# Optimization experiments

Measured on AMD Instinct MI355X. Metric: run time of the kernel, lower is better.

## Reference

```python
import jax, jax.numpy as jnp
import numpy as np

H = 64  # hidden size
IN = 4  # input size


def _lstm_cell(h, c, xt, w_ih, w_hh, b):
    # PyTorch gate order: i, f, g, o
    gates = xt @ w_ih.T + h @ w_hh.T + b  # [B, 4H]
    i, f, g, o = jnp.split(gates, 4, axis=-1)
    i = jax.nn.sigmoid(i)
    f = jax.nn.sigmoid(f)
    g = jnp.tanh(g)
    o = jax.nn.sigmoid(o)
    c = f * c + i * g
    h = o * jnp.tanh(c)
    return h, c


def setup_inputs() -> dict:
    key = jax.random.key(0)
    ks = jax.random.split(key, 12)
    B, T = 512, 1000
    s = 1.0 / np.sqrt(H)  # PyTorch LSTM/Linear init scale
    u = lambda k, shape: jax.random.uniform(k, shape, jnp.float32, -s, s)
    return {
        "x": jax.random.normal(ks[0], (B, T, IN), jnp.float32),
        "w_ih_f": u(ks[1], (4 * H, IN)),
        "w_hh_f": u(ks[2], (4 * H, H)),
        "b_ih_f": u(ks[3], (4 * H,)),
        "b_hh_f": u(ks[4], (4 * H,)),
        "w_ih_b": u(ks[5], (4 * H, IN)),
        "w_hh_b": u(ks[6], (4 * H, H)),
        "b_ih_b": u(ks[7], (4 * H,)),
        "b_hh_b": u(ks[8], (4 * H,)),
        "w_fc": u(ks[9], (1, 2 * H)),
        "b_fc": u(ks[10], (1,)),
    }


def reference(x, w_ih_f, w_hh_f, b_ih_f, b_hh_f,
              w_ih_b, w_hh_b, b_ih_b, b_hh_b, w_fc, b_fc):
    B = x.shape[0]
    # Forward-direction LSTM: only the final hidden state is consumed
    # (out[:, -1, :64] == h_fwd after the last step).
    b_f = b_ih_f + b_hh_f

    def step(carry, xt):
        h, c = carry
        h, c = _lstm_cell(h, c, xt, w_ih_f, w_hh_f, b_f)
        return (h, c), None

    init = (jnp.zeros((B, H), x.dtype), jnp.zeros((B, H), x.dtype))
    xs = jnp.swapaxes(x, 0, 1)  # [T, B, IN]
    (h_fwd, _), _ = jax.lax.scan(step, init, xs)

    # Backward-direction output at the LAST timestep is the backward LSTM's
    # FIRST step (it processes the sequence reversed from zero state):
    # out[:, -1, 64:] == cell(0, 0, x[:, -1]).
    b_b = b_ih_b + b_hh_b
    h0 = jnp.zeros((B, H), x.dtype)
    h_bwd, _ = _lstm_cell(h0, h0, x[:, -1, :], w_ih_b, w_hh_b, b_b)

    last = jnp.concatenate([h_fwd, h_bwd], axis=-1)  # [B, 128]
    # Dropout is identity in eval mode.
    logits = last @ w_fc.T + b_fc  # [B, 1]
    return jax.nn.sigmoid(logits)[:, 0]
```

## Files before the change

### kernel.cpp

```cpp
#include <hip/hip_runtime.h>

#define HDIM 64

typedef _Float16 h2  __attribute__((ext_vector_type(2)));
typedef __fp16   fp2 __attribute__((ext_vector_type(2)));

#if defined(__has_builtin)
# if __has_builtin(__builtin_amdgcn_fdot2)
#  define FDOT2(a, b, c) __builtin_amdgcn_fdot2((a), (b), (c), false)
# endif
#endif
#ifndef FDOT2
__device__ __forceinline__ float fdot2_asm(h2 a, h2 b, float c) {
    float d;
    asm("v_dot2_f32_f16 %0, %1, %2, %3" : "=v"(d) : "v"(a), "v"(b), "v"(c));
    return d;
}
# define FDOT2(a, b, c) fdot2_asm((a), (b), (c))
#endif

__device__ __forceinline__ float fast_sigmoid(float v) {
    return __builtin_amdgcn_rcpf(1.0f + __builtin_amdgcn_exp2f(-1.442695041f * v));
}

__device__ __forceinline__ float fast_tanh(float v) {
    return 1.0f - 2.0f * __builtin_amdgcn_rcpf(1.0f + __builtin_amdgcn_exp2f(2.885390082f * v));
}

__global__ __launch_bounds__(128)
__attribute__((amdgpu_waves_per_eu(1, 1)))
void bilstm_kernel(const float* __restrict__ x,
                   const float* __restrict__ w_ih_f,
                   const float* __restrict__ w_hh_f,
                   const float* __restrict__ b_ih_f,
                   const float* __restrict__ b_hh_f,
                   const float* __restrict__ w_ih_b,
                   const float* __restrict__ b_ih_b,
                   const float* __restrict__ b_hh_b,
                   const float* __restrict__ w_fc,
                   const float* __restrict__ b_fc,
                   float* __restrict__ out,
                   int T)
{
    const int b   = blockIdx.x;
    const int tid = threadIdx.x;
    const int w   = tid >> 6;
    const int l   = tid & 63;

    __shared__ __align__(8)  float2 gbuf[2][2][HDIM];
    __shared__ __align__(16) float  xstage[2][256];

    const int r0 = (w << 7) | l;
    const int r1 = r0 + 64;
    unsigned wu[64];
    #pragma unroll
    for (int g = 0; g < 2; ++g) {
        const float* row = w_hh_f + (size_t)(g ? r1 : r0) * HDIM;
        #pragma unroll
        for (int q = 0; q < 16; ++q) {
            float4 v = *(const float4*)(row + 4 * q);
            fp2 p0 = __builtin_amdgcn_cvt_pkrtz(v.x, v.y);
            fp2 p1 = __builtin_amdgcn_cvt_pkrtz(v.z, v.w);
            wu[(g << 5) + 2 * q + 0] = __builtin_bit_cast(unsigned, p0);
            wu[(g << 5) + 2 * q + 1] = __builtin_bit_cast(unsigned, p1);
        }
    }
    #define PIN_WU()                                                        \
        _Pragma("unroll")                                                   \
        for (int qq = 0; qq < 8; ++qq) {                                    \
            asm volatile("" : "+v"(wu[8*qq+0]), "+v"(wu[8*qq+1]),           \
                              "+v"(wu[8*qq+2]), "+v"(wu[8*qq+3]),           \
                              "+v"(wu[8*qq+4]), "+v"(wu[8*qq+5]),           \
                              "+v"(wu[8*qq+6]), "+v"(wu[8*qq+7]));          \
        }
    PIN_WU()

    float4 wx0 = *(const float4*)(w_ih_f + (size_t)r0 * 4);
    float4 wx1 = *(const float4*)(w_ih_f + (size_t)r1 * 4);
    float  bz0 = b_ih_f[r0] + b_hh_f[r0];
    float  bz1 = b_ih_f[r1] + b_hh_f[r1];
    asm volatile("" : "+v"(wx0.x), "+v"(wx0.y), "+v"(wx0.z), "+v"(wx0.w), "+v"(bz0));
    asm volatile("" : "+v"(wx1.x), "+v"(wx1.y), "+v"(wx1.z), "+v"(wx1.w), "+v"(bz1));

    const float* xb = x + (size_t)b * T * 4;
    const int lim = T * 4 - 1;

    {
        int i0 = tid;        if (i0 > lim) i0 = lim;
        int i1 = tid + 128;  if (i1 > lim) i1 = lim;
        xstage[0][tid]       = xb[i0];
        xstage[0][tid + 128] = xb[i1];
    }
    __syncthreads();

    unsigned hs[32];
    #pragma unroll
    for (int k = 0; k < 32; ++k) hs[k] = 0u;
    float c = 0.0f, h = 0.0f;

    #define W2(g, pp) __builtin_bit_cast(h2, wu[((g) << 5) + (pp)])
    #define H2(u)     __builtin_bit_cast(h2, (u))

    const int NCH = (T + 63) >> 6;

    for (int ch = 0; ch < NCH; ++ch) {
        const int nst = ((T - (ch << 6)) < 64) ? (T - (ch << 6)) : 64;
        const float* xs = xstage[ch & 1];
        const bool more = (ch + 1 < NCH);
        float xn0 = 0.0f, xn1 = 0.0f;
        if (more) {
            int i0 = ((ch + 1) << 8) + tid;        if (i0 > lim) i0 = lim;
            int i1 = ((ch + 1) << 8) + tid + 128;  if (i1 > lim) i1 = lim;
            xn0 = xb[i0];
            xn1 = xb[i1];
        }

        #define STEP(S, P) do {                                              \
            const float4 xt = *(const float4*)(&xs[(S) << 2]);               \
            float a0A = bz0, a0B = 0.0f, a1A = bz1, a1B = 0.0f;              \
            _Pragma("unroll")                                                \
            for (int q = 0; q < 8; ++q) {                                    \
                a0A = FDOT2(W2(0, 4*q+0), H2(hs[4*q+0]), a0A);               \
                a0B = FDOT2(W2(0, 4*q+1), H2(hs[4*q+1]), a0B);               \
                a0A = FDOT2(W2(0, 4*q+2), H2(hs[4*q+2]), a0A);               \
                a0B = FDOT2(W2(0, 4*q+3), H2(hs[4*q+3]), a0B);               \
                a1A = FDOT2(W2(1, 4*q+0), H2(hs[4*q+0]), a1A);               \
                a1B = FDOT2(W2(1, 4*q+1), H2(hs[4*q+1]), a1B);               \
                a1A = FDOT2(W2(1, 4*q+2), H2(hs[4*q+2]), a1A);               \
                a1B = FDOT2(W2(1, 4*q+3), H2(hs[4*q+3]), a1B);               \
            }                                                                \
            const float A0 = a0A + a0B + (wx0.x * xt.x + wx0.y * xt.y        \
                                        + wx0.z * xt.z + wx0.w * xt.w);      \
            const float A1 = a1A + a1B + (wx1.x * xt.x + wx1.y * xt.y        \
                                        + wx1.z * xt.z + wx1.w * xt.w);      \
            float s0, s1;                                                    \
            if (w == 0) { s0 = fast_sigmoid(A0); s1 = fast_sigmoid(A1); }    \
            else        { s0 = fast_tanh(A0);    s1 = fast_sigmoid(A1); }    \
            gbuf[P][w][l] = make_float2(s0, s1);                             \
            __syncthreads();                                                 \
            const float2 ov = gbuf[P][w ^ 1][l];                             \
            float gi, gf, gg, go;                                            \
            if (w == 0) { gi = s0; gf = s1; gg = ov.x; go = ov.y; }          \
            else        { gi = ov.x; gf = ov.y; gg = s0; go = s1; }          \
            c = gf * c + gi * gg;                                            \
            h = go * fast_tanh(c);                                           \
            const unsigned hr = __builtin_bit_cast(unsigned,                 \
                                    __builtin_amdgcn_cvt_pkrtz(h, h));       \
            const unsigned nb = (unsigned)__builtin_amdgcn_update_dpp(       \
                                    (int)hr, (int)hr, 0xB1, 0xF, 0xF, true); \
            const unsigned pk = (hr & 0xffffu) | (nb << 16);                 \
            _Pragma("unroll")                                                \
            for (int k = 0; k < 32; ++k)                                     \
                hs[k] = (unsigned)__builtin_amdgcn_readlane((int)pk, 2 * k); \
        } while (0)

        for (int s = 0; s < nst; s += 2) {
            STEP(s,     0);
            STEP(s + 1, 1);
        }
        #undef STEP

        if (more) {
            xstage[(ch + 1) & 1][tid]       = xn0;
            xstage[(ch + 1) & 1][tid + 128] = xn1;
            __syncthreads();
        }
    }

    #undef W2
    #undef H2
    #undef PIN_WU

    if (w == 0) {
        float4 xl = *(const float4*)(xb + 4 * (T - 1));
        float gb[4];
        #pragma unroll
        for (int g = 0; g < 4; ++g) {
            const int r = (g << 6) | l;
            float4 wb = *(const float4*)(w_ih_b + (size_t)r * 4);
            gb[g] = b_ih_b[r] + b_hh_b[r]
                  + wb.x * xl.x + wb.y * xl.y + wb.z * xl.z + wb.w * xl.w;
        }
        const float ib  = fast_sigmoid(gb[0]);
        const float ggb = fast_tanh(gb[2]);
        const float ob  = fast_sigmoid(gb[3]);
        const float cb  = ib * ggb;
        const float hbk = ob * fast_tanh(cb);

        float p = w_fc[l] * h + w_fc[HDIM + l] * hbk;
        #pragma unroll
        for (int off = 32; off; off >>= 1) p += __shfl_xor(p, off);

        if (l == 0) out[b] = fast_sigmoid(p + b_fc[0]);
    }
}

extern "C" void kernel_launch(void* const* d_in, const int* in_sizes, int n_in,
                              void* d_out, int out_size, void* d_ws, size_t ws_size,
                              hipStream_t stream) {
    const float* x      = (const float*)d_in[0];
    const float* w_ih_f = (const float*)d_in[1];
    const float* w_hh_f = (const float*)d_in[2];
    const float* b_ih_f = (const float*)d_in[3];
    const float* b_hh_f = (const float*)d_in[4];
    const float* w_ih_b = (const float*)d_in[5];
    const float* b_ih_b = (const float*)d_in[7];
    const float* b_hh_b = (const float*)d_in[8];
    const float* w_fc   = (const float*)d_in[9];
    const float* b_fc   = (const float*)d_in[10];
    float* out = (float*)d_out;

    const int B = out_size;
    const int T = in_sizes[0] / (B * 4);

    bilstm_kernel<<<dim3(B), dim3(128), 0, stream>>>(
        x, w_ih_f, w_hh_f, b_ih_f, b_hh_f,
        w_ih_b, b_ih_b, b_hh_b, w_fc, b_fc, out, T);
}
```

Baseline: 405.5 us.

## Split LSTM gates across four waves, one gate row per thread

Measured after the change: 416.3 us. +2.7%, slower.

```diff
diff --git a/kernel.cpp b/kernel.cpp
--- a/kernel.cpp
+++ b/kernel.cpp
@@ -27,8 +27,8 @@
     return 1.0f - 2.0f * __builtin_amdgcn_rcpf(1.0f + __builtin_amdgcn_exp2f(2.885390082f * v));
 }
 
-__global__ __launch_bounds__(128)
-__attribute__((amdgpu_waves_per_eu(1, 1)))
+__global__ __launch_bounds__(256)
+__attribute__((amdgpu_waves_per_eu(2, 2)))
 void bilstm_kernel(const float* __restrict__ x,
                    const float* __restrict__ w_ih_f,
                    const float* __restrict__ w_hh_f,
@@ -44,30 +44,28 @@
 {
     const int b   = blockIdx.x;
     const int tid = threadIdx.x;
-    const int w   = tid >> 6;
+    const int g   = tid >> 6;
     const int l   = tid & 63;
-
-    __shared__ __align__(8)  float2 gbuf[2][2][HDIM];
-    __shared__ __align__(16) float  xstage[2][256];
-
-    const int r0 = (w << 7) | l;
-    const int r1 = r0 + 64;
-    unsigned wu[64];
-    #pragma unroll
-    for (int g = 0; g < 2; ++g) {
-        const float* row = w_hh_f + (size_t)(g ? r1 : r0) * HDIM;
+    const int r   = (g << 6) | l;
+
+    __shared__ float abuf[2][4][HDIM];
+    __shared__ float xstage[2][256];
+
+    unsigned wu[32];
+    {
+        const float* row = w_hh_f + (size_t)r * HDIM;
         #pragma unroll
         for (int q = 0; q < 16; ++q) {
             float4 v = *(const float4*)(row + 4 * q);
             fp2 p0 = __builtin_amdgcn_cvt_pkrtz(v.x, v.y);
             fp2 p1 = __builtin_amdgcn_cvt_pkrtz(v.z, v.w);
-            wu[(g << 5) + 2 * q + 0] = __builtin_bit_cast(unsigned, p0);
-            wu[(g << 5) + 2 * q + 1] = __builtin_bit_cast(unsigned, p1);
+            wu[2 * q + 0] = __builtin_bit_cast(unsigned, p0);
+            wu[2 * q + 1] = __builtin_bit_cast(unsigned, p1);
         }
     }
     #define PIN_WU()                                                        \
         _Pragma("unroll")                                                   \
-        for (int qq = 0; qq < 8; ++qq) {                                    \
+        for (int qq = 0; qq < 4; ++qq) {                                    \
             asm volatile("" : "+v"(wu[8*qq+0]), "+v"(wu[8*qq+1]),           \
                               "+v"(wu[8*qq+2]), "+v"(wu[8*qq+3]),           \
                               "+v"(wu[8*qq+4]), "+v"(wu[8*qq+5]),           \
@@ -75,21 +73,18 @@
         }
     PIN_WU()
 
-    float4 wx0 = *(const float4*)(w_ih_f + (size_t)r0 * 4);
-    float4 wx1 = *(const float4*)(w_ih_f + (size_t)r1 * 4);
-    float  bz0 = b_ih_f[r0] + b_hh_f[r0];
-    float  bz1 = b_ih_f[r1] + b_hh_f[r1];
-    asm volatile("" : "+v"(wx0.x), "+v"(wx0.y), "+v"(wx0.z), "+v"(wx0.w), "+v"(bz0));
-    asm volatile("" : "+v"(wx1.x), "+v"(wx1.y), "+v"(wx1.z), "+v"(wx1.w), "+v"(bz1));
+    float4 wxf = *(const float4*)(w_ih_f + (size_t)r * 4);
+    float  bz  = b_ih_f[r] + b_hh_f[r];
+    asm volatile("" : "+v"(wxf.x), "+v"(wxf.y), "+v"(wxf.z), "+v"(wxf.w), "+v"(bz));
+
+    const float sc = (g == 2) ? 2.885390082f : -1.442695041f;
 
     const float* xb = x + (size_t)b * T * 4;
     const int lim = T * 4 - 1;
 
     {
-        int i0 = tid;        if (i0 > lim) i0 = lim;
-        int i1 = tid + 128;  if (i1 > lim) i1 = lim;
-        xstage[0][tid]       = xb[i0];
-        xstage[0][tid + 128] = xb[i1];
+        int idx = tid;  if (idx > lim) idx = lim;
+        xstage[0][tid] = xb[idx];
     }
     __syncthreads();
 
@@ -98,8 +93,8 @@
     for (int k = 0; k < 32; ++k) hs[k] = 0u;
     float c = 0.0f, h = 0.0f;
 
-    #define W2(g, pp) __builtin_bit_cast(h2, wu[((g) << 5) + (pp)])
-    #define H2(u)     __builtin_bit_cast(h2, (u))
+    #define W2(pp) __builtin_bit_cast(h2, wu[pp])
+    #define H2(u)  __builtin_bit_cast(h2, (u))
 
     const int NCH = (T + 63) >> 6;
 
@@ -107,41 +102,33 @@
         const int nst = ((T - (ch << 6)) < 64) ? (T - (ch << 6)) : 64;
         const float* xs = xstage[ch & 1];
         const bool more = (ch + 1 < NCH);
-        float xn0 = 0.0f, xn1 = 0.0f;
+        float xnf = 0.0f;
         if (more) {
-            int i0 = ((ch + 1) << 8) + tid;        if (i0 > lim) i0 = lim;
-            int i1 = ((ch + 1) << 8) + tid + 128;  if (i1 > lim) i1 = lim;
-            xn0 = xb[i0];
-            xn1 = xb[i1];
+            int idx = ((ch + 1) << 8) + tid;  if (idx > lim) idx = lim;
+            xnf = xb[idx];
         }
 
         #define STEP(S, P) do {                                              \
             const float4 xt = *(const float4*)(&xs[(S) << 2]);               \
-            float a0A = bz0, a0B = 0.0f, a1A = bz1, a1B = 0.0f;              \
+            float aA = bz, aB = 0.0f;                                        \
             _Pragma("unroll")                                                \
             for (int q = 0; q < 8; ++q) {                                    \
-                a0A = FDOT2(W2(0, 4*q+0), H2(hs[4*q+0]), a0A);               \
-                a0B = FDOT2(W2(0, 4*q+1), H2(hs[4*q+1]), a0B);               \
-                a0A = FDOT2(W2(0, 4*q+2), H2(hs[4*q+2]), a0A);               \
-                a0B = FDOT2(W2(0, 4*q+3), H2(hs[4*q+3]), a0B);               \
-                a1A = FDOT2(W2(1, 4*q+0), H2(hs[4*q+0]), a1A);               \
-                a1B = FDOT2(W2(1, 4*q+1), H2(hs[4*q+1]), a1B);               \
-                a1A = FDOT2(W2(1, 4*q+2), H2(hs[4*q+2]), a1A);               \
-                a1B = FDOT2(W2(1, 4*q+3), H2(hs[4*q+3]), a1B);               \
+                aA = FDOT2(W2(4*q+0), H2(hs[4*q+0]), aA);                    \
+                aB = FDOT2(W2(4*q+1), H2(hs[4*q+1]), aB);                    \
+                aA = FDOT2(W2(4*q+2), H2(hs[4*q+2]), aA);                    \
+                aB = FDOT2(W2(4*q+3), H2(hs[4*q+3]), aB);                    \
             }                                                                \
-            const float A0 = a0A + a0B + (wx0.x * xt.x + wx0.y * xt.y        \
-                                        + wx0.z * xt.z + wx0.w * xt.w);      \
-            const float A1 = a1A + a1B + (wx1.x * xt.x + wx1.y * xt.y        \
-                                        + wx1.z * xt.z + wx1.w * xt.w);      \
-            float s0, s1;                                                    \
-            if (w == 0) { s0 = fast_sigmoid(A0); s1 = fast_sigmoid(A1); }    \
-            else        { s0 = fast_tanh(A0);    s1 = fast_sigmoid(A1); }    \
-            gbuf[P][w][l] = make_float2(s0, s1);                             \
+            const float A = aA + aB + (wxf.x * xt.x + wxf.y * xt.y           \
+                                     + wxf.z * xt.z + wxf.w * xt.w);         \
+            const float e  = __builtin_amdgcn_exp2f(sc * A);                 \
+            const float rr = __builtin_amdgcn_rcpf(1.0f + e);                \
+            const float v  = (g == 2) ? 1.0f - 2.0f * rr : rr;               \
+            abuf[P][g][l] = v;                                               \
             __syncthreads();                                                 \
-            const float2 ov = gbuf[P][w ^ 1][l];                             \
-            float gi, gf, gg, go;                                            \
-            if (w == 0) { gi = s0; gf = s1; gg = ov.x; go = ov.y; }          \
-            else        { gi = ov.x; gf = ov.y; gg = s0; go = s1; }          \
+            const float gi = abuf[P][0][l];                                  \
+            const float gf = abuf[P][1][l];                                  \
+            const float gg = abuf[P][2][l];                                  \
+            const float go = abuf[P][3][l];                                  \
             c = gf * c + gi * gg;                                            \
             h = go * fast_tanh(c);                                           \
             const unsigned hr = __builtin_bit_cast(unsigned,                 \
@@ -161,8 +148,7 @@
         #undef STEP
 
         if (more) {
-            xstage[(ch + 1) & 1][tid]       = xn0;
-            xstage[(ch + 1) & 1][tid + 128] = xn1;
+            xstage[(ch + 1) & 1][tid] = xnf;
             __syncthreads();
         }
     }
@@ -171,15 +157,15 @@
     #undef H2
     #undef PIN_WU
 
-    if (w == 0) {
+    if (g == 0) {
         float4 xl = *(const float4*)(xb + 4 * (T - 1));
         float gb[4];
         #pragma unroll
-        for (int g = 0; g < 4; ++g) {
-            const int r = (g << 6) | l;
-            float4 wb = *(const float4*)(w_ih_b + (size_t)r * 4);
-            gb[g] = b_ih_b[r] + b_hh_b[r]
-                  + wb.x * xl.x + wb.y * xl.y + wb.z * xl.z + wb.w * xl.w;
+        for (int jj = 0; jj < 4; ++jj) {
+            const int rr2 = (jj << 6) | l;
+            float4 wb = *(const float4*)(w_ih_b + (size_t)rr2 * 4);
+            gb[jj] = b_ih_b[rr2] + b_hh_b[rr2]
+                   + wb.x * xl.x + wb.y * xl.y + wb.z * xl.z + wb.w * xl.w;
         }
         const float ib  = fast_sigmoid(gb[0]);
         const float ggb = fast_tanh(gb[2]);
@@ -213,7 +199,7 @@
     const int B = out_size;
     const int T = in_sizes[0] / (B * 4);
 
-    bilstm_kernel<<<dim3(B), dim3(128), 0, stream>>>(
+    bilstm_kernel<<<dim3(B), dim3(256), 0, stream>>>(
         x, w_ih_f, w_hh_f, b_ih_f, b_hh_f,
         w_ih_b, b_ih_b, b_hh_b, w_fc, b_fc, out, T);
 }
```
